# Performance work log

Hardware: AMD Instinct MI355X
Metric: run time of the kernel (lower is better)

## Reference

```python
import jax, jax.numpy as jnp
import numpy as np

B, T, D_MODEL, N_HEAD = 8, 1024, 1024, 8
D_K = D_MODEL // N_HEAD  # = d_v = 128; V projection shared across heads


def setup_inputs() -> dict:
    key = jax.random.key(0)
    ks = jax.random.split(key, 8)
    scale = 0.02
    q = jax.random.normal(ks[0], (B, T, D_MODEL), jnp.float32)
    k = jax.random.normal(ks[1], (B, T, D_MODEL), jnp.float32)
    v = jax.random.normal(ks[2], (B, T, D_MODEL), jnp.float32)
    # causal mask, 1.0 = attend, broadcast to batch (shape (B, T, T))
    mask = jnp.broadcast_to(jnp.tril(jnp.ones((T, T), jnp.float32)), (B, T, T))
    Wq = jax.random.normal(ks[3], (N_HEAD, D_MODEL, D_K), jnp.float32) * scale
    Wk = jax.random.normal(ks[4], (N_HEAD, D_MODEL, D_K), jnp.float32) * scale
    Wv = jax.random.normal(ks[5], (D_MODEL, D_K), jnp.float32) * scale  # shared across heads
    Wo = jax.random.normal(ks[6], (D_K, D_MODEL), jnp.float32) * scale
    return {"q": q, "k": k, "v": v, "mask": mask, "Wq": Wq, "Wk": Wk, "Wv": Wv, "Wo": Wo}


def reference(q, k, v, mask, Wq, Wk, Wv, Wo):
    # Per-head Q/K projections (batched over heads), shared V projection.
    qh = jnp.einsum('btd,hdk->hbtk', q, Wq)  # (H,B,T,d_k)
    kh = jnp.einsum('bsd,hdk->hbsk', k, Wk)  # (H,B,S,d_k)
    vh = jnp.einsum('bsd,dk->bsk', v, Wv)    # (B,S,d_v) shared across heads
    temper = jnp.sqrt(jnp.asarray(qh.shape[-1], jnp.float32))
    scores = jnp.einsum('hbtk,hbsk->hbts', qh, kh) / temper
    scores = scores + (-1e9) * (1.0 - mask)[None]  # additive mask per head
    attn = jax.nn.softmax(scores, axis=-1)          # (H,B,T,S)
    heads = jnp.einsum('hbts,bsk->hbtk', attn, vh)  # (H,B,T,d_v)
    out = jnp.einsum('btk,kd->btd', heads.mean(axis=0), Wo)  # mean over heads, then w_o
    return out, attn  # dropout rate 0.0 / inference -> identity
```

## Files before the change

kernel.cpp:

```cpp
#include <hip/hip_runtime.h>
#include <cstdint>

typedef __attribute__((ext_vector_type(8))) short bf16x8;
typedef __attribute__((ext_vector_type(4))) float f32x4;

constexpr int NH = 8, NB = 8, SEQ = 1024, DM = 1024, DK = 128;
constexpr int MTOT = NB * SEQ;

__device__ __forceinline__ unsigned short f2bf(float f) {
    unsigned int u = __float_as_uint(f);
    unsigned int r = (u + 0x7fffu + ((u >> 16) & 1u)) >> 16;
    return (unsigned short)r;
}
__device__ __forceinline__ float bf2f(unsigned int s) {
    return __uint_as_float((s & 0xffffu) << 16);
}
__device__ __forceinline__ void gld16(const void* g, void* l) {
    __builtin_amdgcn_global_load_lds((const __attribute__((address_space(1))) void*)g,
                                     (__attribute__((address_space(3))) void*)l, 16, 0, 0);
}

__global__ __launch_bounds__(256) void transpose_w_kernel(
    const float* __restrict__ Wq, const float* __restrict__ Wk,
    const float* __restrict__ Wv, const float* __restrict__ Wo,
    unsigned short* __restrict__ WqT, unsigned short* __restrict__ WkT,
    unsigned short* __restrict__ WvT, unsigned short* __restrict__ WoT)
{
    const int s = blockIdx.y;
    const float* in; unsigned short* out; int R, C;
    if (s < 8)        { in = Wq + (size_t)s * DM * DK;       out = WqT + (size_t)s * DK * DM;       R = DM; C = DK; }
    else if (s < 16)  { in = Wk + (size_t)(s - 8) * DM * DK; out = WkT + (size_t)(s - 8) * DK * DM; R = DM; C = DK; }
    else if (s == 16) { in = Wv; out = WvT; R = DM; C = DK; }
    else              { in = Wo; out = WoT; R = DK; C = DM; }
    const int tc = C / 32;
    const int r0 = (blockIdx.x / tc) * 32, c0 = (blockIdx.x % tc) * 32;
    __shared__ unsigned short t[32][33];
    const int tid = threadIdx.x;
    const int a = tid >> 3, b4 = (tid & 7) * 4;
    float4 f = *reinterpret_cast<const float4*>(&in[(size_t)(r0 + a) * C + c0 + b4]);
    t[a][b4 + 0] = f2bf(f.x); t[a][b4 + 1] = f2bf(f.y);
    t[a][b4 + 2] = f2bf(f.z); t[a][b4 + 3] = f2bf(f.w);
    __syncthreads();
    ushort4 o;
    o.x = t[b4 + 0][a]; o.y = t[b4 + 1][a]; o.z = t[b4 + 2][a]; o.w = t[b4 + 3][a];
    *reinterpret_cast<ushort4*>(&out[(size_t)(c0 + a) * R + r0 + b4]) = o;
}

__global__ __launch_bounds__(256) void cvt_kernel(
    const float* __restrict__ q, const float* __restrict__ k, const float* __restrict__ v,
    unsigned short* __restrict__ qb, unsigned short* __restrict__ kb,
    unsigned short* __restrict__ vb)
{
    const float* src; unsigned short* dst;
    const int s = blockIdx.y;
    if (s == 0)      { src = q; dst = qb; }
    else if (s == 1) { src = k; dst = kb; }
    else             { src = v; dst = vb; }
    const size_t base = ((size_t)blockIdx.x * 256 + threadIdx.x) * 8;
    float4 f0 = *reinterpret_cast<const float4*>(&src[base]);
    float4 f1 = *reinterpret_cast<const float4*>(&src[base + 4]);
    uint4 o;
    o.x = (unsigned int)f2bf(f0.x) | ((unsigned int)f2bf(f0.y) << 16);
    o.y = (unsigned int)f2bf(f0.z) | ((unsigned int)f2bf(f0.w) << 16);
    o.z = (unsigned int)f2bf(f1.x) | ((unsigned int)f2bf(f1.y) << 16);
    o.w = (unsigned int)f2bf(f1.z) | ((unsigned int)f2bf(f1.w) << 16);
    *reinterpret_cast<uint4*>(&dst[base]) = o;
}

__global__ __launch_bounds__(256) void proj_kernel(
    const unsigned short* __restrict__ qb, const unsigned short* __restrict__ kb,
    const unsigned short* __restrict__ vb,
    const unsigned short* __restrict__ WqT, const unsigned short* __restrict__ WkT,
    const unsigned short* __restrict__ WvT,
    unsigned short* __restrict__ qh, unsigned short* __restrict__ kh,
    unsigned short* __restrict__ vt)
{
    const int g = blockIdx.x, m0 = blockIdx.y * 128;
    const unsigned short* Ab; const unsigned short* Bt;
    if (g < 8)       { Ab = qb; Bt = WqT + (size_t)g * DK * DM; }
    else if (g < 16) { Ab = kb; Bt = WkT + (size_t)(g - 8) * DK * DM; }
    else             { Ab = vb; Bt = WvT; }

    __shared__ unsigned short As[2][128][32];
    __shared__ unsigned short Bs[2][128][32];

    const int tid = threadIdx.x, wave = tid >> 6, lane = tid & 63, quad = lane >> 4, l15 = lane & 15;
    const int wm = (wave & 1) * 64, wn = (wave >> 1) * 64;

    f32x4 acc[4][4];
    for (int mi = 0; mi < 4; ++mi)
        for (int ni = 0; ni < 4; ++ni)
            acc[mi][ni] = (f32x4){0.f, 0.f, 0.f, 0.f};

    const int s_row = tid >> 2;
    const int s_col = ((tid & 3) ^ ((s_row >> 1) & 3)) * 8;
    const unsigned short* gA = Ab + (size_t)(m0 + s_row) * DM + s_col;
    const unsigned short* gAh = Ab + (size_t)(m0 + 64 + s_row) * DM + s_col;
    const unsigned short* gB = Bt + (size_t)s_row * DM + s_col;
    const unsigned short* gBh = Bt + (size_t)(64 + s_row) * DM + s_col;
    char* lA = (char*)&As[0][0][0] + wave * 1024;
    char* lB = (char*)&Bs[0][0][0] + wave * 1024;
    const int rcb = (quad ^ ((l15 >> 1) & 3)) * 8;

    auto STAGE = [&](int k0, int bsel) {
        gld16(gA + k0, lA + bsel * 8192);
        gld16(gAh + k0, lA + bsel * 8192 + 4096);
        gld16(gB + k0, lB + bsel * 8192);
        gld16(gBh + k0, lB + bsel * 8192 + 4096);
    };

    int bsel = 0;
    STAGE(0, 0);
    __syncthreads();
    for (int k0 = 0; k0 < DM; k0 += 32) {
        if (k0 + 32 < DM) STAGE(k0 + 32, bsel ^ 1);
        bf16x8 af[4], bfr[4];
        for (int mi = 0; mi < 4; ++mi)
            af[mi] = *reinterpret_cast<const bf16x8*>(&As[bsel][wm + mi * 16 + l15][rcb]);
        for (int ni = 0; ni < 4; ++ni)
            bfr[ni] = *reinterpret_cast<const bf16x8*>(&Bs[bsel][wn + ni * 16 + l15][rcb]);
        for (int mi = 0; mi < 4; ++mi)
            for (int ni = 0; ni < 4; ++ni)
                acc[mi][ni] = __builtin_amdgcn_mfma_f32_16x16x32_bf16(af[mi], bfr[ni], acc[mi][ni], 0, 0, 0);
        __syncthreads();
        bsel ^= 1;
    }

    if (g < 16) {
        unsigned short* C = (g < 8) ? (qh + (size_t)g * MTOT * DK)
                                    : (kh + (size_t)(g - 8) * MTOT * DK);
        for (int mi = 0; mi < 4; ++mi)
            for (int ni = 0; ni < 4; ++ni)
                for (int r = 0; r < 4; ++r)
                    C[(size_t)(m0 + wm + mi * 16 + quad * 4 + r) * DK + wn + ni * 16 + l15] =
                        f2bf(acc[mi][ni][r]);
    } else {
        for (int mi = 0; mi < 4; ++mi)
            for (int ni = 0; ni < 4; ++ni)
                for (int r = 0; r < 4; ++r) {
                    int row = m0 + wm + mi * 16 + quad * 4 + r;
                    int col = wn + ni * 16 + l15;
                    vt[((size_t)(row >> 10) * DK + col) * SEQ + (row & 1023)] = f2bf(acc[mi][ni][r]);
                }
    }
}

__global__ __launch_bounds__(512, 4) void attn_kernel(
    const unsigned short* __restrict__ qh, const unsigned short* __restrict__ kh,
    const unsigned short* __restrict__ vt, unsigned short* __restrict__ heads,
    float* __restrict__ attn)
{
    const int id = blockIdx.y * 8 + blockIdx.x;
    const int hi = (id >> 8) & 1;
    const int p  = ((id & 7) + hi * 4) & 7;
    const int hb = hi * 32 + ((id >> 3) & 31);
    const int b  = hb & 7;

    const int tid = threadIdx.x;
    const int wg = tid >> 8;
    const int lt = tid & 255;
    const int w8 = tid >> 6;
    const int lw = w8 & 3;
    const int lane = tid & 63, quad = lane >> 4, l15 = lane & 15;

    const int ti = wg ? (15 - p) : p;
    const int JMAX = 15 - p;

    const unsigned short* kbase = kh + (size_t)hb * SEQ * DK;
    const unsigned short* vbase = vt + (size_t)b * DK * SEQ;
    const unsigned short* qbase = qh + ((size_t)hb * SEQ + ti * 64) * DK;
    float* attn_base            = attn + ((size_t)hb * SEQ + ti * 64) * SEQ;
    unsigned short* hbase       = heads + ((size_t)hb * SEQ + ti * 64) * DK;

    __shared__ unsigned short Ks[2][4][64][32];
    __shared__ unsigned short Ps[2][64][72];

    const float scale = 0.08838834764831843f;

    const int s_rg  = w8 & 3;
    const int s_ks0 = w8 >> 2;
    const int s_row = s_rg * 16 + (lane >> 2);
    const int s_col = ((lane & 3) ^ ((s_row >> 1) & 3)) * 8;
    const unsigned short* gK = kbase + (size_t)s_row * DK + s_col;
    char* d0base = (char*)&Ks[0][s_ks0][s_rg * 16][0];
    char* d1base = (char*)&Ks[0][s_ks0 + 2][s_rg * 16][0];

    auto STAGE = [&](int j, int bsel) {
        const unsigned short* src = gK + (size_t)j * 64 * DK;
        gld16(src + s_ks0 * 32, d0base + bsel * 16384);
        gld16(src + (s_ks0 + 2) * 32, d1base + bsel * 16384);
    };

    const int rcb = (quad ^ ((l15 >> 1) & 3)) * 8;

    bf16x8 aq[4];
    for (int ks = 0; ks < 4; ++ks)
        aq[ks] = *reinterpret_cast<const bf16x8*>(
            &qbase[(size_t)(lw * 16 + l15) * DK + ks * 32 + quad * 8]);

    const int trow_base = ti * 64 + lw * 16 + quad * 4;
    float l_run[4] = {0.f, 0.f, 0.f, 0.f};

    int bsel = 0;
    STAGE(0, 0);
    __syncthreads();
    for (int j = 0; j <= JMAX; ++j) {
        if (j < JMAX) STAGE(j + 1, bsel ^ 1);
        if (j <= ti) {
            f32x4 sacc[4];
            for (int ni = 0; ni < 4; ++ni) sacc[ni] = (f32x4){0.f, 0.f, 0.f, 0.f};
            for (int ks = 0; ks < 4; ++ks)
                for (int ni = 0; ni < 4; ++ni) {
                    bf16x8 bb = *reinterpret_cast<const bf16x8*>(&Ks[bsel][ks][ni * 16 + l15][rcb]);
                    sacc[ni] = __builtin_amdgcn_mfma_f32_16x16x32_bf16(aq[ks], bb, sacc[ni], 0, 0, 0);
                }
            const bool diag = (j == ti);
            for (int r = 0; r < 4; ++r) {
                float lsum = 0.f;
                for (int ni = 0; ni < 4; ++ni) {
                    int s = j * 64 + ni * 16 + l15;
                    float e = __expf(sacc[ni][r] * scale);
                    lsum += (!diag || s <= trow_base + r) ? e : 0.f;
                }
                for (int off = 1; off < 16; off <<= 1)
                    lsum += __shfl_xor(lsum, off, 64);
                l_run[r] += lsum;
            }
        }
        __syncthreads();
        bsel ^= 1;
    }

    float inv_l[4];
    for (int r = 0; r < 4; ++r) inv_l[r] = 1.f / l_run[r];
    f32x4 oacc[8];
    for (int n = 0; n < 8; ++n) oacc[n] = (f32x4){0.f, 0.f, 0.f, 0.f};

    STAGE(0, bsel);
    __syncthreads();
    for (int j = 0; j <= JMAX; ++j) {
        if (j < JMAX) STAGE(j + 1, bsel ^ 1);
        if (j <= ti) {
            f32x4 sacc[4];
            for (int ni = 0; ni < 4; ++ni) sacc[ni] = (f32x4){0.f, 0.f, 0.f, 0.f};
            for (int ks = 0; ks < 4; ++ks)
                for (int ni = 0; ni < 4; ++ni) {
                    bf16x8 bb = *reinterpret_cast<const bf16x8*>(&Ks[bsel][ks][ni * 16 + l15][rcb]);
                    sacc[ni] = __builtin_amdgcn_mfma_f32_16x16x32_bf16(aq[ks], bb, sacc[ni], 0, 0, 0);
                }
            const bool diag = (j == ti);
            for (int r = 0; r < 4; ++r)
                for (int ni = 0; ni < 4; ++ni) {
                    int s = j * 64 + ni * 16 + l15;
                    float pv = (!diag || s <= trow_base + r)
                                  ? __expf(sacc[ni][r] * scale) * inv_l[r] : 0.f;
                    __builtin_nontemporal_store(
                        pv, &attn_base[(size_t)(lw * 16 + quad * 4 + r) * SEQ + s]);
                    Ps[wg][lw * 16 + quad * 4 + r][ni * 16 + l15] = f2bf(pv);
                }
            for (int ks2 = 0; ks2 < 2; ++ks2) {
                bf16x8 ap = *reinterpret_cast<const bf16x8*>(&Ps[wg][lw * 16 + l15][ks2 * 32 + quad * 8]);
                for (int n2 = 0; n2 < 8; ++n2) {
                    bf16x8 bv = *reinterpret_cast<const bf16x8*>(
                        &vbase[(size_t)(n2 * 16 + l15) * SEQ + j * 64 + ks2 * 32 + quad * 8]);
                    oacc[n2] = __builtin_amdgcn_mfma_f32_16x16x32_bf16(ap, bv, oacc[n2], 0, 0, 0);
                }
            }
        }
        __syncthreads();
        bsel ^= 1;
    }

    for (int n2 = 0; n2 < 8; ++n2)
        for (int r = 0; r < 4; ++r)
            hbase[(size_t)(lw * 16 + quad * 4 + r) * DK + n2 * 16 + l15] = f2bf(oacc[n2][r]);

    {
        const int s0 = (ti + 1) * 64;
        if (s0 < SEQ) {
            const int z4 = (SEQ - s0) >> 2;
            f32x4 zz = {0.f, 0.f, 0.f, 0.f};
            for (int r = 0; r < 64; ++r)
                for (int c = lt; c < z4; c += 256)
                    __builtin_nontemporal_store(zz, (f32x4*)&attn_base[(size_t)r * SEQ + s0 + c * 4]);
        }
    }
}

__global__ __launch_bounds__(256) void mean_kernel(
    const unsigned short* __restrict__ heads, unsigned short* __restrict__ hmean)
{
    size_t base = ((size_t)blockIdx.x * 256 + threadIdx.x) * 8;
    float s[8] = {0.f, 0.f, 0.f, 0.f, 0.f, 0.f, 0.f, 0.f};
    for (int h = 0; h < 8; ++h) {
        uint4 u = *reinterpret_cast<const uint4*>(&heads[(size_t)h * MTOT * DK + base]);
        s[0] += bf2f(u.x); s[1] += bf2f(u.x >> 16);
        s[2] += bf2f(u.y); s[3] += bf2f(u.y >> 16);
        s[4] += bf2f(u.z); s[5] += bf2f(u.z >> 16);
        s[6] += bf2f(u.w); s[7] += bf2f(u.w >> 16);
    }
    uint4 o;
    o.x = (unsigned int)f2bf(s[0] * 0.125f) | ((unsigned int)f2bf(s[1] * 0.125f) << 16);
    o.y = (unsigned int)f2bf(s[2] * 0.125f) | ((unsigned int)f2bf(s[3] * 0.125f) << 16);
    o.z = (unsigned int)f2bf(s[4] * 0.125f) | ((unsigned int)f2bf(s[5] * 0.125f) << 16);
    o.w = (unsigned int)f2bf(s[6] * 0.125f) | ((unsigned int)f2bf(s[7] * 0.125f) << 16);
    *reinterpret_cast<uint4*>(&hmean[base]) = o;
}

__global__ __launch_bounds__(256) void out_kernel(
    const unsigned short* __restrict__ hmean, const unsigned short* __restrict__ WoT,
    float* __restrict__ out)
{
    const int n0 = blockIdx.x * 128, m0 = blockIdx.y * 128;
    __shared__ unsigned short As[128][32];
    __shared__ unsigned short Bs[128][32];

    const int tid = threadIdx.x, wave = tid >> 6, lane = tid & 63, quad = lane >> 4, l15 = lane & 15;
    const int wm = (wave & 1) * 64, wn = (wave >> 1) * 64;

    f32x4 acc[4][4];
    for (int mi = 0; mi < 4; ++mi)
        for (int ni = 0; ni < 4; ++ni)
            acc[mi][ni] = (f32x4){0.f, 0.f, 0.f, 0.f};

    const unsigned short* gA0 = hmean + (size_t)(m0 + (tid >> 2)) * DK + (tid & 3) * 8;
    const unsigned short* gB0 = WoT + (size_t)(n0 + (tid >> 2)) * DK + (tid & 3) * 8;
    char* lA = (char*)&As[0][0] + wave * 1024;
    char* lB = (char*)&Bs[0][0] + wave * 1024;

    for (int k0 = 0; k0 < DK; k0 += 32) {
        __syncthreads();
        gld16(gA0 + k0, lA); gld16(gA0 + k0 + 64 * DK, lA + 4096);
        gld16(gB0 + k0, lB); gld16(gB0 + k0 + 64 * DK, lB + 4096);
        __syncthreads();
        bf16x8 af[4], bfr[4];
        for (int mi = 0; mi < 4; ++mi)
            af[mi] = *reinterpret_cast<const bf16x8*>(&As[wm + mi * 16 + l15][quad * 8]);
        for (int ni = 0; ni < 4; ++ni)
            bfr[ni] = *reinterpret_cast<const bf16x8*>(&Bs[wn + ni * 16 + l15][quad * 8]);
        for (int mi = 0; mi < 4; ++mi)
            for (int ni = 0; ni < 4; ++ni)
                acc[mi][ni] = __builtin_amdgcn_mfma_f32_16x16x32_bf16(af[mi], bfr[ni], acc[mi][ni], 0, 0, 0);
    }
    for (int mi = 0; mi < 4; ++mi)
        for (int ni = 0; ni < 4; ++ni)
            for (int r = 0; r < 4; ++r)
                out[(size_t)(m0 + wm + mi * 16 + quad * 4 + r) * DM + n0 + wn + ni * 16 + l15] =
                    acc[mi][ni][r];
}

extern "C" void kernel_launch(void* const* d_in, const int* in_sizes, int n_in,
                              void* d_out, int out_size, void* d_ws, size_t ws_size,
                              hipStream_t stream) {
    (void)in_sizes; (void)n_in; (void)out_size; (void)ws_size;
    const float* q  = (const float*)d_in[0];
    const float* k  = (const float*)d_in[1];
    const float* v  = (const float*)d_in[2];
    const float* Wq = (const float*)d_in[4];
    const float* Wk = (const float*)d_in[5];
    const float* Wv = (const float*)d_in[6];
    const float* Wo = (const float*)d_in[7];

    float* out  = (float*)d_out;
    float* attn = out + (size_t)NB * SEQ * DM;
    unsigned short* heads = (unsigned short*)d_out;
    unsigned short* qb = (unsigned short*)attn;
    unsigned short* kb = qb + (size_t)MTOT * DM;
    unsigned short* vb = kb + (size_t)MTOT * DM;

    unsigned short* ws    = (unsigned short*)d_ws;
    unsigned short* WqT   = ws;
    unsigned short* WkT   = WqT + (size_t)NH * DK * DM;
    unsigned short* WvT   = WkT + (size_t)NH * DK * DM;
    unsigned short* WoT   = WvT + (size_t)DK * DM;
    unsigned short* qh    = WoT + (size_t)DM * DK;
    unsigned short* kh    = qh + (size_t)NH * MTOT * DK;
    unsigned short* vt    = kh + (size_t)NH * MTOT * DK;
    unsigned short* hmean = vt + (size_t)NB * DK * SEQ;

    transpose_w_kernel<<<dim3(128, 18), 256, 0, stream>>>(Wq, Wk, Wv, Wo, WqT, WkT, WvT, WoT);
    cvt_kernel<<<dim3(4096, 3), 256, 0, stream>>>(q, k, v, qb, kb, vb);
    proj_kernel<<<dim3(17, 64), 256, 0, stream>>>(qb, kb, vb, WqT, WkT, WvT, qh, kh, vt);
    attn_kernel<<<dim3(8, 64), 512, 0, stream>>>(qh, kh, vt, heads, attn);
    mean_kernel<<<512, 256, 0, stream>>>(heads, hmean);
    out_kernel<<<dim3(8, 64), 256, 0, stream>>>(hmean, WoT, out);
}
```

Baseline: 615.1 us.

## Split attention into separate row-sum and PV kernels with LDS-staged V

The fused two-pass attention kernel, which paired complementary causal tiles in 512-thread blocks, becomes two kernels. The first computes the softmax row-sum inverses and writes them to workspace; the second recomputes the scores, writes the attention probabilities and accumulates P·V. V tiles are now staged into swizzled LDS with async global-to-LDS loads instead of being read directly from global memory. Block scheduling uses a slot-to-tile mapping to balance causal work. The cost is an extra launch and a global round trip for the inverse sums, and blocks no longer carry balanced paired work.

After: 569.3 us. -7.4%, faster.

```diff
diff --git a/kernel.cpp b/kernel.cpp
--- a/kernel.cpp
+++ b/kernel.cpp
@@ -18,6 +18,10 @@
 __device__ __forceinline__ void gld16(const void* g, void* l) {
     __builtin_amdgcn_global_load_lds((const __attribute__((address_space(1))) void*)g,
                                      (__attribute__((address_space(3))) void*)l, 16, 0, 0);
+}
+__device__ __forceinline__ int ti_of_slot(int v) {
+    int u = v & 3, s2 = v >> 2;
+    return (s2 == 0) ? u : (s2 == 1) ? (15 - u) : (s2 == 2) ? (8 + u) : (7 - u);
 }
 
 __global__ __launch_bounds__(256) void transpose_w_kernel(
@@ -145,26 +149,86 @@
     }
 }
 
-__global__ __launch_bounds__(512, 4) void attn_kernel(
+__global__ __launch_bounds__(256) void attn_lse_kernel(
     const unsigned short* __restrict__ qh, const unsigned short* __restrict__ kh,
-    const unsigned short* __restrict__ vt, unsigned short* __restrict__ heads,
-    float* __restrict__ attn)
-{
-    const int id = blockIdx.y * 8 + blockIdx.x;
-    const int hi = (id >> 8) & 1;
-    const int p  = ((id & 7) + hi * 4) & 7;
-    const int hb = hi * 32 + ((id >> 3) & 31);
-    const int b  = hb & 7;
-
-    const int tid = threadIdx.x;
-    const int wg = tid >> 8;
-    const int lt = tid & 255;
-    const int w8 = tid >> 6;
-    const int lw = w8 & 3;
-    const int lane = tid & 63, quad = lane >> 4, l15 = lane & 15;
-
-    const int ti = wg ? (15 - p) : p;
-    const int JMAX = 15 - p;
+    float* __restrict__ linv)
+{
+    const int hb = blockIdx.x;
+    const int ti = ti_of_slot(blockIdx.y);
+
+    const unsigned short* kbase = kh + (size_t)hb * SEQ * DK;
+    const unsigned short* qbase = qh + ((size_t)hb * SEQ + ti * 64) * DK;
+
+    __shared__ unsigned short Ks[2][4][64][32];
+
+    const int tid = threadIdx.x, wave = tid >> 6, lane = tid & 63, quad = lane >> 4, l15 = lane & 15;
+    const float scale = 0.08838834764831843f;
+
+    int koff[4]; char* kdst[4];
+#pragma unroll
+    for (int i = 0; i < 4; ++i) {
+        int slot = wave * 256 + i * 64 + lane;
+        int ks = slot >> 8, row = (slot >> 2) & 63;
+        int c = (slot & 3) ^ ((row >> 1) & 3);
+        koff[i] = row * DK + ks * 32 + c * 8;
+        kdst[i] = (char*)&Ks[0][0][0][0] + slot * 16;
+    }
+    auto STAGE = [&](int j, int bsel) {
+        const unsigned short* src = kbase + (size_t)j * 64 * DK;
+#pragma unroll
+        for (int i = 0; i < 4; ++i) gld16(src + koff[i], kdst[i] + bsel * 16384);
+    };
+
+    const int rcb = (quad ^ ((l15 >> 1) & 3)) * 8;
+
+    bf16x8 aq[4];
+    for (int ks = 0; ks < 4; ++ks)
+        aq[ks] = *reinterpret_cast<const bf16x8*>(
+            &qbase[(size_t)(wave * 16 + l15) * DK + ks * 32 + quad * 8]);
+
+    const int trow_base = ti * 64 + wave * 16 + quad * 4;
+    float l_run[4] = {0.f, 0.f, 0.f, 0.f};
+
+    int bsel = 0;
+    STAGE(0, 0);
+    __syncthreads();
+    for (int j = 0; j <= ti; ++j) {
+        if (j < ti) STAGE(j + 1, bsel ^ 1);
+        f32x4 sacc[4];
+        for (int ni = 0; ni < 4; ++ni) sacc[ni] = (f32x4){0.f, 0.f, 0.f, 0.f};
+        for (int ks = 0; ks < 4; ++ks)
+            for (int ni = 0; ni < 4; ++ni) {
+                bf16x8 bb = *reinterpret_cast<const bf16x8*>(&Ks[bsel][ks][ni * 16 + l15][rcb]);
+                sacc[ni] = __builtin_amdgcn_mfma_f32_16x16x32_bf16(aq[ks], bb, sacc[ni], 0, 0, 0);
+            }
+        const bool diag = (j == ti);
+        for (int r = 0; r < 4; ++r) {
+            float lsum = 0.f;
+            for (int ni = 0; ni < 4; ++ni) {
+                int s = j * 64 + ni * 16 + l15;
+                float e = __expf(sacc[ni][r] * scale);
+                lsum += (!diag || s <= trow_base + r) ? e : 0.f;
+            }
+            for (int off = 1; off < 16; off <<= 1)
+                lsum += __shfl_xor(lsum, off, 64);
+            l_run[r] += lsum;
+        }
+        __syncthreads();
+        bsel ^= 1;
+    }
+
+    if (l15 == 0)
+        for (int r = 0; r < 4; ++r)
+            linv[(size_t)hb * SEQ + ti * 64 + wave * 16 + quad * 4 + r] = 1.f / l_run[r];
+}
+
+__global__ __launch_bounds__(256) void attn_pv_kernel(
+    const unsigned short* __restrict__ qh, const unsigned short* __restrict__ kh,
+    const unsigned short* __restrict__ vt, const float* __restrict__ linv,
+    unsigned short* __restrict__ heads, float* __restrict__ attn)
+{
+    const int hb = blockIdx.x, b = hb & 7;
+    const int ti = ti_of_slot(blockIdx.y);
 
     const unsigned short* kbase = kh + (size_t)hb * SEQ * DK;
     const unsigned short* vbase = vt + (size_t)b * DK * SEQ;
@@ -173,107 +237,92 @@
     unsigned short* hbase       = heads + ((size_t)hb * SEQ + ti * 64) * DK;
 
     __shared__ unsigned short Ks[2][4][64][32];
-    __shared__ unsigned short Ps[2][64][72];
-
+    __shared__ unsigned short Vs[2][128][64];
+    __shared__ unsigned short Ps[64][72];
+
+    const int tid = threadIdx.x, wave = tid >> 6, lane = tid & 63, quad = lane >> 4, l15 = lane & 15;
     const float scale = 0.08838834764831843f;
 
-    const int s_rg  = w8 & 3;
-    const int s_ks0 = w8 >> 2;
-    const int s_row = s_rg * 16 + (lane >> 2);
-    const int s_col = ((lane & 3) ^ ((s_row >> 1) & 3)) * 8;
-    const unsigned short* gK = kbase + (size_t)s_row * DK + s_col;
-    char* d0base = (char*)&Ks[0][s_ks0][s_rg * 16][0];
-    char* d1base = (char*)&Ks[0][s_ks0 + 2][s_rg * 16][0];
-
+    int koff[4]; char* kdst[4]; int voff[4]; char* vdst[4];
+#pragma unroll
+    for (int i = 0; i < 4; ++i) {
+        int slot = wave * 256 + i * 64 + lane;
+        {
+            int ks = slot >> 8, row = (slot >> 2) & 63;
+            int c = (slot & 3) ^ ((row >> 1) & 3);
+            koff[i] = row * DK + ks * 32 + c * 8;
+            kdst[i] = (char*)&Ks[0][0][0][0] + slot * 16;
+        }
+        {
+            int row = slot >> 3;
+            int c = (slot & 7) ^ (row & 7);
+            voff[i] = row * SEQ + c * 8;
+            vdst[i] = (char*)&Vs[0][0][0] + slot * 16;
+        }
+    }
     auto STAGE = [&](int j, int bsel) {
-        const unsigned short* src = gK + (size_t)j * 64 * DK;
-        gld16(src + s_ks0 * 32, d0base + bsel * 16384);
-        gld16(src + (s_ks0 + 2) * 32, d1base + bsel * 16384);
+        const unsigned short* srcK = kbase + (size_t)j * 64 * DK;
+        const unsigned short* srcV = vbase + j * 64;
+#pragma unroll
+        for (int i = 0; i < 4; ++i) {
+            gld16(srcK + koff[i], kdst[i] + bsel * 16384);
+            gld16(srcV + voff[i], vdst[i] + bsel * 16384);
+        }
     };
 
     const int rcb = (quad ^ ((l15 >> 1) & 3)) * 8;
+    const int vxor = l15 & 7;
 
     bf16x8 aq[4];
     for (int ks = 0; ks < 4; ++ks)
         aq[ks] = *reinterpret_cast<const bf16x8*>(
-            &qbase[(size_t)(lw * 16 + l15) * DK + ks * 32 + quad * 8]);
-
-    const int trow_base = ti * 64 + lw * 16 + quad * 4;
-    float l_run[4] = {0.f, 0.f, 0.f, 0.f};
+            &qbase[(size_t)(wave * 16 + l15) * DK + ks * 32 + quad * 8]);
+
+    float inv_l[4];
+    for (int r = 0; r < 4; ++r)
+        inv_l[r] = linv[(size_t)hb * SEQ + ti * 64 + wave * 16 + quad * 4 + r];
+
+    const int trow_base = ti * 64 + wave * 16 + quad * 4;
+    f32x4 oacc[8];
+    for (int n = 0; n < 8; ++n) oacc[n] = (f32x4){0.f, 0.f, 0.f, 0.f};
 
     int bsel = 0;
     STAGE(0, 0);
     __syncthreads();
-    for (int j = 0; j <= JMAX; ++j) {
-        if (j < JMAX) STAGE(j + 1, bsel ^ 1);
-        if (j <= ti) {
-            f32x4 sacc[4];
-            for (int ni = 0; ni < 4; ++ni) sacc[ni] = (f32x4){0.f, 0.f, 0.f, 0.f};
-            for (int ks = 0; ks < 4; ++ks)
-                for (int ni = 0; ni < 4; ++ni) {
-                    bf16x8 bb = *reinterpret_cast<const bf16x8*>(&Ks[bsel][ks][ni * 16 + l15][rcb]);
-                    sacc[ni] = __builtin_amdgcn_mfma_f32_16x16x32_bf16(aq[ks], bb, sacc[ni], 0, 0, 0);
-                }
-            const bool diag = (j == ti);
-            for (int r = 0; r < 4; ++r) {
-                float lsum = 0.f;
-                for (int ni = 0; ni < 4; ++ni) {
-                    int s = j * 64 + ni * 16 + l15;
-                    float e = __expf(sacc[ni][r] * scale);
-                    lsum += (!diag || s <= trow_base + r) ? e : 0.f;
-                }
-                for (int off = 1; off < 16; off <<= 1)
-                    lsum += __shfl_xor(lsum, off, 64);
-                l_run[r] += lsum;
+    for (int j = 0; j <= ti; ++j) {
+        if (j < ti) STAGE(j + 1, bsel ^ 1);
+        f32x4 sacc[4];
+        for (int ni = 0; ni < 4; ++ni) sacc[ni] = (f32x4){0.f, 0.f, 0.f, 0.f};
+        for (int ks = 0; ks < 4; ++ks)
+            for (int ni = 0; ni < 4; ++ni) {
+                bf16x8 bb = *reinterpret_cast<const bf16x8*>(&Ks[bsel][ks][ni * 16 + l15][rcb]);
+                sacc[ni] = __builtin_amdgcn_mfma_f32_16x16x32_bf16(aq[ks], bb, sacc[ni], 0, 0, 0);
+            }
+        const bool diag = (j == ti);
+        for (int r = 0; r < 4; ++r)
+            for (int ni = 0; ni < 4; ++ni) {
+                int s = j * 64 + ni * 16 + l15;
+                float pv = (!diag || s <= trow_base + r)
+                              ? __expf(sacc[ni][r] * scale) * inv_l[r] : 0.f;
+                __builtin_nontemporal_store(
+                    pv, &attn_base[(size_t)(wave * 16 + quad * 4 + r) * SEQ + s]);
+                Ps[wave * 16 + quad * 4 + r][ni * 16 + l15] = f2bf(pv);
+            }
+        for (int ks2 = 0; ks2 < 2; ++ks2) {
+            bf16x8 ap = *reinterpret_cast<const bf16x8*>(&Ps[wave * 16 + l15][ks2 * 32 + quad * 8]);
+            const int c = (ks2 * 4 + quad) ^ vxor;
+            for (int n2 = 0; n2 < 8; ++n2) {
+                bf16x8 bv = *reinterpret_cast<const bf16x8*>(&Vs[bsel][n2 * 16 + l15][c * 8]);
+                oacc[n2] = __builtin_amdgcn_mfma_f32_16x16x32_bf16(ap, bv, oacc[n2], 0, 0, 0);
             }
         }
         __syncthreads();
         bsel ^= 1;
     }
 
-    float inv_l[4];
-    for (int r = 0; r < 4; ++r) inv_l[r] = 1.f / l_run[r];
-    f32x4 oacc[8];
-    for (int n = 0; n < 8; ++n) oacc[n] = (f32x4){0.f, 0.f, 0.f, 0.f};
-
-    STAGE(0, bsel);
-    __syncthreads();
-    for (int j = 0; j <= JMAX; ++j) {
-        if (j < JMAX) STAGE(j + 1, bsel ^ 1);
-        if (j <= ti) {
-            f32x4 sacc[4];
-            for (int ni = 0; ni < 4; ++ni) sacc[ni] = (f32x4){0.f, 0.f, 0.f, 0.f};
-            for (int ks = 0; ks < 4; ++ks)
-                for (int ni = 0; ni < 4; ++ni) {
-                    bf16x8 bb = *reinterpret_cast<const bf16x8*>(&Ks[bsel][ks][ni * 16 + l15][rcb]);
-                    sacc[ni] = __builtin_amdgcn_mfma_f32_16x16x32_bf16(aq[ks], bb, sacc[ni], 0, 0, 0);
-                }
-            const bool diag = (j == ti);
-            for (int r = 0; r < 4; ++r)
-                for (int ni = 0; ni < 4; ++ni) {
-                    int s = j * 64 + ni * 16 + l15;
-                    float pv = (!diag || s <= trow_base + r)
-                                  ? __expf(sacc[ni][r] * scale) * inv_l[r] : 0.f;
-                    __builtin_nontemporal_store(
-                        pv, &attn_base[(size_t)(lw * 16 + quad * 4 + r) * SEQ + s]);
-                    Ps[wg][lw * 16 + quad * 4 + r][ni * 16 + l15] = f2bf(pv);
-                }
-            for (int ks2 = 0; ks2 < 2; ++ks2) {
-                bf16x8 ap = *reinterpret_cast<const bf16x8*>(&Ps[wg][lw * 16 + l15][ks2 * 32 + quad * 8]);
-                for (int n2 = 0; n2 < 8; ++n2) {
-                    bf16x8 bv = *reinterpret_cast<const bf16x8*>(
-                        &vbase[(size_t)(n2 * 16 + l15) * SEQ + j * 64 + ks2 * 32 + quad * 8]);
-                    oacc[n2] = __builtin_amdgcn_mfma_f32_16x16x32_bf16(ap, bv, oacc[n2], 0, 0, 0);
-                }
-            }
-        }
-        __syncthreads();
-        bsel ^= 1;
-    }
-
     for (int n2 = 0; n2 < 8; ++n2)
         for (int r = 0; r < 4; ++r)
-            hbase[(size_t)(lw * 16 + quad * 4 + r) * DK + n2 * 16 + l15] = f2bf(oacc[n2][r]);
+            hbase[(size_t)(wave * 16 + quad * 4 + r) * DK + n2 * 16 + l15] = f2bf(oacc[n2][r]);
 
     {
         const int s0 = (ti + 1) * 64;
@@ -281,7 +330,7 @@
             const int z4 = (SEQ - s0) >> 2;
             f32x4 zz = {0.f, 0.f, 0.f, 0.f};
             for (int r = 0; r < 64; ++r)
-                for (int c = lt; c < z4; c += 256)
+                for (int c = tid; c < z4; c += 256)
                     __builtin_nontemporal_store(zz, (f32x4*)&attn_base[(size_t)r * SEQ + s0 + c * 4]);
         }
     }
@@ -377,11 +426,13 @@
     unsigned short* kh    = qh + (size_t)NH * MTOT * DK;
     unsigned short* vt    = kh + (size_t)NH * MTOT * DK;
     unsigned short* hmean = vt + (size_t)NB * DK * SEQ;
+    float* linv           = (float*)(hmean + (size_t)MTOT * DK);
 
     transpose_w_kernel<<<dim3(128, 18), 256, 0, stream>>>(Wq, Wk, Wv, Wo, WqT, WkT, WvT, WoT);
     cvt_kernel<<<dim3(4096, 3), 256, 0, stream>>>(q, k, v, qb, kb, vb);
     proj_kernel<<<dim3(17, 64), 256, 0, stream>>>(qb, kb, vb, WqT, WkT, WvT, qh, kh, vt);
-    attn_kernel<<<dim3(8, 64), 512, 0, stream>>>(qh, kh, vt, heads, attn);
+    attn_lse_kernel<<<dim3(64, 16), 256, 0, stream>>>(qh, kh, linv);
+    attn_pv_kernel<<<dim3(64, 16), 256, 0, stream>>>(qh, kh, vt, linv, heads, attn);
     mean_kernel<<<512, 256, 0, stream>>>(heads, hmean);
     out_kernel<<<dim3(8, 64), 256, 0, stream>>>(hmean, WoT, out);
 }
```
